# Kernel optimization log

Measured on AMD Instinct MI355X. Metric: run time of the kernel, lower is better.

Reference implementation:

```python
import jax, jax.numpy as jnp
import numpy as np

CLIP_LIMIT = 40.0
GRID = (8, 8)
NUM_BINS = 256


def setup_inputs() -> dict:
    key = jax.random.key(0)
    x = jax.random.uniform(key, (2, 3, 2048, 2048), dtype=jnp.float32)
    return {"x": x}


def _clahe(x, clip_limit=CLIP_LIMIT, grid=GRID, num_bins=NUM_BINS):
    B, C, H, W = x.shape
    gh, gw = grid
    th = -(-H // gh)          # ceil(H / gh) tile height
    tw = -(-W // gw)          # tile width
    pad_h = th * gh - H
    pad_w = tw * gw - W
    if pad_h or pad_w:
        xp = jnp.pad(x, ((0, 0), (0, 0), (0, pad_h), (0, pad_w)), mode="reflect")
    else:
        xp = x
    Hp, Wp = th * gh, tw * gw
    pixels = th * tw

    # ---- per-tile histograms (scatter-add) ----
    # tiles: (B*C*gh*gw, th*tw)
    tiles = xp.reshape(B, C, gh, th, gw, tw).transpose(0, 1, 2, 4, 3, 5).reshape(-1, pixels)
    T = tiles.shape[0]
    bins = jnp.clip(jnp.floor(tiles * num_bins), 0, num_bins - 1).astype(jnp.int32)
    flat = (jnp.arange(T, dtype=jnp.int32)[:, None] * num_bins + bins).reshape(-1)
    histos = jax.ops.segment_sum(
        jnp.ones((T * pixels,), jnp.float32), flat, num_segments=T * num_bins
    ).reshape(T, num_bins)

    # ---- clip + uniform redistribution of excess ----
    if clip_limit > 0.0:
        max_val = max(int(clip_limit * pixels) // num_bins, 1)
        clipped = jnp.minimum(histos, float(max_val))
        excess = pixels - clipped.sum(axis=1, keepdims=True)  # >= 0
        histos = clipped + excess / num_bins

    # ---- CDF -> LUT (values in [0, num_bins-1], floored like kornia) ----
    lut_scale = (num_bins - 1) / pixels
    luts = jnp.floor(jnp.clip(jnp.cumsum(histos, axis=1) * lut_scale, 0.0, num_bins - 1.0))
    luts = luts.reshape(B, C, gh, gw, num_bins)

    # ---- per-pixel bilinear interpolation across the 4 neighbouring tile LUTs ----
    ys = jnp.clip((jnp.arange(Hp, dtype=jnp.float32) + 0.5) / th - 0.5, 0.0, gh - 1.0)
    xs = jnp.clip((jnp.arange(Wp, dtype=jnp.float32) + 0.5) / tw - 0.5, 0.0, gw - 1.0)
    y0 = jnp.floor(ys).astype(jnp.int32)
    x0 = jnp.floor(xs).astype(jnp.int32)
    y1 = jnp.minimum(y0 + 1, gh - 1)
    x1 = jnp.minimum(x0 + 1, gw - 1)
    wy = (ys - y0.astype(jnp.float32))[None, None, :, None]
    wx = (xs - x0.astype(jnp.float32))[None, None, None, :]

    pbin = jnp.clip(jnp.floor(xp * (num_bins - 1)), 0, num_bins - 1).astype(jnp.int32)
    bi = jnp.arange(B)[:, None, None, None]
    ci = jnp.arange(C)[None, :, None, None]
    Y0 = y0[None, None, :, None]; Y1 = y1[None, None, :, None]
    X0 = x0[None, None, None, :]; X1 = x1[None, None, None, :]

    v00 = luts[bi, ci, Y0, X0, pbin]
    v01 = luts[bi, ci, Y0, X1, pbin]
    v10 = luts[bi, ci, Y1, X0, pbin]
    v11 = luts[bi, ci, Y1, X1, pbin]

    out = ((1.0 - wy) * ((1.0 - wx) * v00 + wx * v01)
           + wy * ((1.0 - wx) * v10 + wx * v11)) / (num_bins - 1)
    return out[..., :H, :W]


def reference(x):
    return _clahe(x)
```

## Files before the change

### kernel.cpp

```cpp
#include <hip/hip_runtime.h>

#define H 2048
#define W 2048
#define NBINS 256
#define NIMG 6
#define NTILE 384
#define IMGPX (H * W)

typedef unsigned int u32;
typedef unsigned char u8;
typedef float f32x4 __attribute__((ext_vector_type(4)));

__global__ __launch_bounds__(256) void clahe_hist(const float* __restrict__ x,
                                                  u32* __restrict__ part,
                                                  u8* __restrict__ pbin) {
    int blk  = blockIdx.x;
    int tile = blk >> 2;
    int q    = blk & 3;
    int tx   = tile & 7;
    int ty   = (tile >> 3) & 7;
    int img  = tile >> 6;
    const float* base = x + (size_t)img * IMGPX;
    u8* pb = pbin + (size_t)img * IMGPX;
    int row0 = ty * 256 + q * 64;
    int col0 = tx * 256;

    __shared__ u32 lh[4][NBINS];
    int t = threadIdx.x;
    for (int i = t; i < 4 * NBINS; i += 256) ((u32*)lh)[i] = 0;
    __syncthreads();

    int w  = t >> 6;
    int cg = t & 63;
    for (int it = 0; it < 16; ++it) {
        int row = row0 + w + 4 * it;
        size_t off = (size_t)row * W + col0 + cg * 4;
        float4 v = *(const float4*)(base + off);
        int b0 = min((int)(v.x * 256.0f), 255);
        int b1 = min((int)(v.y * 256.0f), 255);
        int b2 = min((int)(v.z * 256.0f), 255);
        int b3 = min((int)(v.w * 256.0f), 255);
        atomicAdd(&lh[w][b0], 1u);
        atomicAdd(&lh[w][b1], 1u);
        atomicAdd(&lh[w][b2], 1u);
        atomicAdd(&lh[w][b3], 1u);
        u32 p0 = min((int)(v.x * 255.0f), 255);
        u32 p1 = min((int)(v.y * 255.0f), 255);
        u32 p2 = min((int)(v.z * 255.0f), 255);
        u32 p3 = min((int)(v.w * 255.0f), 255);
        *(u32*)(pb + off) = p0 | (p1 << 8) | (p2 << 16) | (p3 << 24);
    }
    __syncthreads();
    part[(size_t)blk * NBINS + t] =
        lh[0][t] + lh[1][t] + lh[2][t] + lh[3][t];
}

__global__ __launch_bounds__(256) void clahe_lut(const u32* __restrict__ part,
                                                 float* __restrict__ luts) {
    int tile = blockIdx.x;
    int t = threadIdx.x;
    const u32* p = part + (size_t)tile * 4 * NBINS;
    float h = (float)(p[t] + p[NBINS + t] + p[2 * NBINS + t] + p[3 * NBINS + t]);
    float v = fminf(h, 10240.0f);

    int lane = t & 63, wid = t >> 6;
    #pragma unroll
    for (int off = 1; off < 64; off <<= 1) {
        float n = __shfl_up(v, off, 64);
        if (lane >= off) v += n;
    }
    __shared__ float wsum[4];
    __shared__ float tot;
    if (lane == 63) wsum[wid] = v;
    __syncthreads();
    float add = 0.0f;
    for (int ww = 0; ww < wid; ++ww) add += wsum[ww];
    v += add;
    if (t == 255) tot = v;
    __syncthreads();

    float e   = (65536.0f - tot) * (1.0f / 256.0f);
    float cum = v + (float)(t + 1) * e;
    float lut = floorf(fminf(fmaxf(cum * (255.0f / 65536.0f), 0.0f), 255.0f));
    luts[(size_t)tile * NBINS + t] = lut * (1.0f / 255.0f);
}

__global__ __launch_bounds__(256) void clahe_apply(const u8* __restrict__ pbin,
                                                   const float* __restrict__ luts,
                                                   float* __restrict__ out) {
    int rx  = blockIdx.x * 128;
    int ry  = blockIdx.y * 64;
    int img = blockIdx.z;

    int yc = ry + 32, xc = rx + 64;
    int y0 = min(max((int)floorf((yc + 0.5f) * (1.0f / 256.0f) - 0.5f), 0), 7);
    int x0 = min(max((int)floorf((xc + 0.5f) * (1.0f / 256.0f) - 0.5f), 0), 7);
    int y1 = min(y0 + 1, 7), x1 = min(x0 + 1, 7);

    const float* lb = luts + (size_t)img * 64 * NBINS;
    __shared__ float l00[NBINS], l01[NBINS], l10[NBINS], l11[NBINS];
    int t = threadIdx.x;
    l00[t] = lb[(y0 * 8 + x0) * NBINS + t];
    l01[t] = lb[(y0 * 8 + x1) * NBINS + t];
    l10[t] = lb[(y1 * 8 + x0) * NBINS + t];
    l11[t] = lb[(y1 * 8 + x1) * NBINS + t];
    __syncthreads();

    const u8* pbase = pbin + (size_t)img * IMGPX;
    float*    obase = out  + (size_t)img * IMGPX;

    int cg = t & 31, rg = t >> 5;
    int col = rx + cg * 4;

    float fx0 = (float)x0;
    float wxa[4];
    #pragma unroll
    for (int k = 0; k < 4; ++k) {
        float xs = (col + k + 0.5f) * (1.0f / 256.0f) - 0.5f;
        xs = fminf(fmaxf(xs, 0.0f), 7.0f);
        wxa[k] = xs - fx0;
    }

    #pragma unroll
    for (int it = 0; it < 8; ++it) {
        int row = ry + rg + 8 * it;
        float ys = (row + 0.5f) * (1.0f / 256.0f) - 0.5f;
        ys = fminf(fmaxf(ys, 0.0f), 7.0f);
        float wy = ys - (float)y0;

        size_t off = (size_t)row * W + col;
        u32 pw = *(const u32*)(pbase + off);

        float r[4];
        #pragma unroll
        for (int k = 0; k < 4; ++k) {
            int p = (pw >> (8 * k)) & 255;
            float wx = wxa[k];
            float ix0 = (1.0f - wx) * l00[p] + wx * l01[p];
            float ix1 = (1.0f - wx) * l10[p] + wx * l11[p];
            r[k] = (1.0f - wy) * ix0 + wy * ix1;
        }
        f32x4 o = {r[0], r[1], r[2], r[3]};
        __builtin_nontemporal_store(o, (f32x4*)(obase + off));
    }
}

extern "C" void kernel_launch(void* const* d_in, const int* in_sizes, int n_in,
                              void* d_out, int out_size, void* d_ws, size_t ws_size,
                              hipStream_t stream) {
    const float* x = (const float*)d_in[0];
    float* out = (float*)d_out;

    const size_t PBIN_BYTES = (size_t)NIMG * IMGPX;
    const size_t PART_BYTES = (size_t)NTILE * 4 * NBINS * 4;

    u8*    pbin = (u8*)d_ws;
    u32*   part = (u32*)((char*)d_ws + PBIN_BYTES);
    float* luts = (float*)((char*)d_ws + PBIN_BYTES + PART_BYTES);

    clahe_hist<<<dim3(NTILE * 4), dim3(256), 0, stream>>>(x, part, pbin);
    clahe_lut<<<dim3(NTILE), dim3(256), 0, stream>>>(part, luts);
    clahe_apply<<<dim3(16, 32, NIMG), dim3(256), 0, stream>>>(pbin, luts, out);
}
```

Before: 53.10 us.

## Fuse LUT build into apply kernel and recompute bins from input

```diff
diff --git a/kernel.cpp b/kernel.cpp
--- a/kernel.cpp
+++ b/kernel.cpp
@@ -12,8 +12,7 @@
 typedef float f32x4 __attribute__((ext_vector_type(4)));
 
 __global__ __launch_bounds__(256) void clahe_hist(const float* __restrict__ x,
-                                                  u32* __restrict__ part,
-                                                  u8* __restrict__ pbin) {
+                                                  u32* __restrict__ part) {
     int blk  = blockIdx.x;
     int tile = blk >> 2;
     int q    = blk & 3;
@@ -21,7 +20,6 @@
     int ty   = (tile >> 3) & 7;
     int img  = tile >> 6;
     const float* base = x + (size_t)img * IMGPX;
-    u8* pb = pbin + (size_t)img * IMGPX;
     int row0 = ty * 256 + q * 64;
     int col0 = tx * 256;
 
@@ -44,49 +42,14 @@
         atomicAdd(&lh[w][b1], 1u);
         atomicAdd(&lh[w][b2], 1u);
         atomicAdd(&lh[w][b3], 1u);
-        u32 p0 = min((int)(v.x * 255.0f), 255);
-        u32 p1 = min((int)(v.y * 255.0f), 255);
-        u32 p2 = min((int)(v.z * 255.0f), 255);
-        u32 p3 = min((int)(v.w * 255.0f), 255);
-        *(u32*)(pb + off) = p0 | (p1 << 8) | (p2 << 16) | (p3 << 24);
     }
     __syncthreads();
     part[(size_t)blk * NBINS + t] =
         lh[0][t] + lh[1][t] + lh[2][t] + lh[3][t];
 }
 
-__global__ __launch_bounds__(256) void clahe_lut(const u32* __restrict__ part,
-                                                 float* __restrict__ luts) {
-    int tile = blockIdx.x;
-    int t = threadIdx.x;
-    const u32* p = part + (size_t)tile * 4 * NBINS;
-    float h = (float)(p[t] + p[NBINS + t] + p[2 * NBINS + t] + p[3 * NBINS + t]);
-    float v = fminf(h, 10240.0f);
-
-    int lane = t & 63, wid = t >> 6;
-    #pragma unroll
-    for (int off = 1; off < 64; off <<= 1) {
-        float n = __shfl_up(v, off, 64);
-        if (lane >= off) v += n;
-    }
-    __shared__ float wsum[4];
-    __shared__ float tot;
-    if (lane == 63) wsum[wid] = v;
-    __syncthreads();
-    float add = 0.0f;
-    for (int ww = 0; ww < wid; ++ww) add += wsum[ww];
-    v += add;
-    if (t == 255) tot = v;
-    __syncthreads();
-
-    float e   = (65536.0f - tot) * (1.0f / 256.0f);
-    float cum = v + (float)(t + 1) * e;
-    float lut = floorf(fminf(fmaxf(cum * (255.0f / 65536.0f), 0.0f), 255.0f));
-    luts[(size_t)tile * NBINS + t] = lut * (1.0f / 255.0f);
-}
-
-__global__ __launch_bounds__(256) void clahe_apply(const u8* __restrict__ pbin,
-                                                   const float* __restrict__ luts,
+__global__ __launch_bounds__(256) void clahe_apply(const float* __restrict__ x,
+                                                   const u32* __restrict__ part,
                                                    float* __restrict__ out) {
     int rx  = blockIdx.x * 128;
     int ry  = blockIdx.y * 64;
@@ -97,17 +60,48 @@
     int x0 = min(max((int)floorf((xc + 0.5f) * (1.0f / 256.0f) - 0.5f), 0), 7);
     int y1 = min(y0 + 1, 7), x1 = min(x0 + 1, 7);
 
-    const float* lb = luts + (size_t)img * 64 * NBINS;
-    __shared__ float l00[NBINS], l01[NBINS], l10[NBINS], l11[NBINS];
+    __shared__ alignas(16) float s_lut[4][NBINS];
+
     int t = threadIdx.x;
-    l00[t] = lb[(y0 * 8 + x0) * NBINS + t];
-    l01[t] = lb[(y0 * 8 + x1) * NBINS + t];
-    l10[t] = lb[(y1 * 8 + x0) * NBINS + t];
-    l11[t] = lb[(y1 * 8 + x1) * NBINS + t];
+    int w = t >> 6, lane = t & 63;
+
+    {
+        int tys = (w & 2) ? y1 : y0;
+        int txs = (w & 1) ? x1 : x0;
+        int tile = (img << 6) | (tys << 3) | txs;
+        const u32* pb = part + (size_t)tile * 4 * NBINS;
+        uint4 q0 = *((const uint4*)(pb) + lane);
+        uint4 q1 = *((const uint4*)(pb + NBINS) + lane);
+        uint4 q2 = *((const uint4*)(pb + 2 * NBINS) + lane);
+        uint4 q3 = *((const uint4*)(pb + 3 * NBINS) + lane);
+        float v0 = fminf((float)(q0.x + q1.x + q2.x + q3.x), 10240.0f);
+        float v1 = fminf((float)(q0.y + q1.y + q2.y + q3.y), 10240.0f);
+        float v2 = fminf((float)(q0.z + q1.z + q2.z + q3.z), 10240.0f);
+        float v3 = fminf((float)(q0.w + q1.w + q2.w + q3.w), 10240.0f);
+        float c0 = v0, c1 = c0 + v1, c2 = c1 + v2, c3 = c2 + v3;
+        float s = c3;
+        #pragma unroll
+        for (int off = 1; off < 64; off <<= 1) {
+            float n = __shfl_up(s, off, 64);
+            if (lane >= off) s += n;
+        }
+        float excl = s - c3;
+        float tot  = __shfl(s, 63, 64);
+        float e = (65536.0f - tot) * (1.0f / 256.0f);
+        int bi = 4 * lane;
+        const float sc = 255.0f / 65536.0f;
+        f32x4 L;
+        L.x = floorf(fminf(fmaxf((excl + c0 + (float)(bi + 1) * e) * sc, 0.0f), 255.0f));
+        L.y = floorf(fminf(fmaxf((excl + c1 + (float)(bi + 2) * e) * sc, 0.0f), 255.0f));
+        L.z = floorf(fminf(fmaxf((excl + c2 + (float)(bi + 3) * e) * sc, 0.0f), 255.0f));
+        L.w = floorf(fminf(fmaxf((excl + c3 + (float)(bi + 4) * e) * sc, 0.0f), 255.0f));
+        L *= (1.0f / 255.0f);
+        ((f32x4*)s_lut[w])[lane] = L;
+    }
     __syncthreads();
 
-    const u8* pbase = pbin + (size_t)img * IMGPX;
-    float*    obase = out  + (size_t)img * IMGPX;
+    const float* base  = x   + (size_t)img * IMGPX;
+    float*       obase = out + (size_t)img * IMGPX;
 
     int cg = t & 31, rg = t >> 5;
     int col = rx + cg * 4;
@@ -129,15 +123,16 @@
         float wy = ys - (float)y0;
 
         size_t off = (size_t)row * W + col;
-        u32 pw = *(const u32*)(pbase + off);
+        float4 v = *(const float4*)(base + off);
+        float vv[4] = {v.x, v.y, v.z, v.w};
 
         float r[4];
         #pragma unroll
         for (int k = 0; k < 4; ++k) {
-            int p = (pw >> (8 * k)) & 255;
+            int p = min((int)(vv[k] * 255.0f), 255);
             float wx = wxa[k];
-            float ix0 = (1.0f - wx) * l00[p] + wx * l01[p];
-            float ix1 = (1.0f - wx) * l10[p] + wx * l11[p];
+            float ix0 = (1.0f - wx) * s_lut[0][p] + wx * s_lut[1][p];
+            float ix1 = (1.0f - wx) * s_lut[2][p] + wx * s_lut[3][p];
             r[k] = (1.0f - wy) * ix0 + wy * ix1;
         }
         f32x4 o = {r[0], r[1], r[2], r[3]};
@@ -151,14 +146,8 @@
     const float* x = (const float*)d_in[0];
     float* out = (float*)d_out;
 
-    const size_t PBIN_BYTES = (size_t)NIMG * IMGPX;
-    const size_t PART_BYTES = (size_t)NTILE * 4 * NBINS * 4;
+    u32* part = (u32*)d_ws;
 
-    u8*    pbin = (u8*)d_ws;
-    u32*   part = (u32*)((char*)d_ws + PBIN_BYTES);
-    float* luts = (float*)((char*)d_ws + PBIN_BYTES + PART_BYTES);
-
-    clahe_hist<<<dim3(NTILE * 4), dim3(256), 0, stream>>>(x, part, pbin);
-    clahe_lut<<<dim3(NTILE), dim3(256), 0, stream>>>(part, luts);
-    clahe_apply<<<dim3(16, 32, NIMG), dim3(256), 0, stream>>>(pbin, luts, out);
+    clahe_hist<<<dim3(NTILE * 4), dim3(256), 0, stream>>>(x, part);
+    clahe_apply<<<dim3(16, 32, NIMG), dim3(256), 0, stream>>>(x, part, out);
 }
```

Result: slower. 59.81 us (+12.6%).
